# Kernel tuning notes

Hardware: AMD Instinct MI355X
Metric: run time of the kernel (lower is better)

Reference implementation:

```python
import jax, jax.numpy as jnp
import numpy as np
from jax import lax

T, B, D_IN, H, D_OUT = 512, 64, 256, 512, 256


def _lstm_scan(xs, h0, c0, Wih, Whh, b):
    """Standard LSTM over time. xs: [T,B,Din]; returns (hs [T,B,H], hT, cT).
    Gate order i,f,g,o (PyTorch convention)."""
    def step(carry, x_t):
        h, c = carry
        gates = x_t @ Wih.T + h @ Whh.T + b            # [B, 4H]
        i, f, g, o = jnp.split(gates, 4, axis=-1)
        i = jax.nn.sigmoid(i)
        f = jax.nn.sigmoid(f)
        g = jnp.tanh(g)
        o = jax.nn.sigmoid(o)
        c = f * c + i * g
        h = o * jnp.tanh(c)
        return (h, c), h
    (hT, cT), hs = lax.scan(step, (h0, c0), xs)
    return hs, hT, cT


def setup_inputs() -> dict:
    key = jax.random.key(0)
    ks = jax.random.split(key, 10)
    s = 0.05
    return {
        "x": jax.random.normal(ks[0], (T, B, D_IN), jnp.float32),
        "target": jax.random.uniform(ks[1], (T, B, D_OUT), jnp.float32),
        "hidden_state": jnp.zeros((1, B, H), jnp.float32),
        "cell_state": jnp.zeros((1, B, H), jnp.float32),
        "enc_Wih": jax.random.normal(ks[2], (4 * H, D_IN), jnp.float32) * s,
        "enc_Whh": jax.random.normal(ks[3], (4 * H, H), jnp.float32) * s,
        "enc_b": jax.random.normal(ks[4], (4 * H,), jnp.float32) * s,
        "dec_Wih": jax.random.normal(ks[5], (4 * H, D_OUT), jnp.float32) * s,
        "dec_Whh": jax.random.normal(ks[6], (4 * H, H), jnp.float32) * s,
        "dec_b": jax.random.normal(ks[7], (4 * H,), jnp.float32) * s,
        "fc_W": jax.random.normal(ks[8], (D_OUT, H), jnp.float32) * s,
        "fc_b": jax.random.normal(ks[9], (D_OUT,), jnp.float32) * s,
    }


def reference(x, target, hidden_state, cell_state,
              enc_Wih, enc_Whh, enc_b, dec_Wih, dec_Whh, dec_b, fc_W, fc_b):
    # Encoder: consume x, keep final (h, c).
    _, h, c = _lstm_scan(x, hidden_state[0], cell_state[0], enc_Wih, enc_Whh, enc_b)
    # Decoder with teacher_forcing = 1.0: input at step t is target[t-1],
    # step 0 input is zeros (matches torch code's initial x = zeros).
    dec_in = jnp.concatenate([jnp.zeros((1,) + target.shape[1:], target.dtype),
                              target[:-1]], axis=0)          # [T, B, D_OUT]
    hs, _, _ = _lstm_scan(dec_in, h, c, dec_Wih, dec_Whh, dec_b)  # [T, B, H]
    logits = hs @ fc_W.T + fc_b                                   # [T, B, D_OUT]
    return jax.nn.softmax(logits, axis=-1)
```

## Files before the change

kernel.cpp:

```cpp
#include <hip/hip_runtime.h>
#include <math.h>

#define TT 512
#define BB 64
#define DIN 256
#define HH 512
#define DOUT 256

#define RSU 388
#define RSH 776

#define W_HI_OFF 0
#define W_LO_OFF 12416
#define A_HI_OFF 24832
#define A_LO_OFF 31040
#define P_OFF    37248
#define B_OFF    38528
#define C_OFF    38560
#define HST_HI   38688
#define HST_LO   38752
#define SMEM_U32 38816
#define SMEM_BYTES (SMEM_U32*4)

#define FCS 516

typedef _Float16 f16x8 __attribute__((ext_vector_type(8)));
typedef float    f32x4 __attribute__((ext_vector_type(4)));
typedef unsigned u32x4 __attribute__((ext_vector_type(4)));

union H16 { _Float16 f; unsigned short u; };
__device__ __forceinline__ unsigned short f16bits(_Float16 h) { H16 t; t.f = h; return t.u; }

__device__ __forceinline__ void pack2(float x, float y, unsigned& hi, unsigned& lo) {
    _Float16 hx = (_Float16)x, hy = (_Float16)y;
    _Float16 lx = (_Float16)((x - (float)hx) * 2048.0f);
    _Float16 ly = (_Float16)((y - (float)hy) * 2048.0f);
    hi = (unsigned)f16bits(hx) | ((unsigned)f16bits(hy) << 16);
    lo = (unsigned)f16bits(lx) | ((unsigned)f16bits(ly) << 16);
}

__device__ __forceinline__ u32x4 ld16_cohere(const void* p) {
    u32x4 v;
    asm volatile("global_load_dwordx4 %0, %1, off sc0 sc1"
                 : "=&v"(v) : "v"(p) : "memory");
    return v;
}
__device__ __forceinline__ void st16_cohere(void* p, u32x4 v) {
    asm volatile("global_store_dwordx4 %0, %1, off sc0 sc1"
                 :: "v"(p), "v"(v) : "memory");
}

__device__ __forceinline__ void load_w_f16(unsigned* __restrict__ sm32, float* __restrict__ b_l,
                                           const float* __restrict__ Whh,
                                           const float* __restrict__ Wih,
                                           const float* __restrict__ bias,
                                           int u0, int tid) {
    for (int r = 0; r < 48; ++r) {
        int id = tid + 256*r;
        int cc = id / 384;
        int jj = id - cc*384;
        int C  = (cc >> 3)*HH + u0 + (cc & 7);
        float2 v;
        if (jj < 256) v = ((const float2*)(Whh + (size_t)C*HH))[jj];
        else          v = ((const float2*)(Wih + (size_t)C*DIN))[jj - 256];
        unsigned hi, lo;
        pack2(v.x, v.y, hi, lo);
        sm32[W_HI_OFF + cc*RSU + jj] = hi;
        sm32[W_LO_OFF + cc*RSU + jj] = lo;
    }
    if (tid < 32) {
        int C = (tid >> 3)*HH + u0 + (tid & 7);
        b_l[tid] = bias[C];
    }
}

__device__ __forceinline__ void stage_x_f16(unsigned* __restrict__ sm32,
                                            const float* __restrict__ src, int tid) {
    for (int r = 0; r < 4; ++r) {
        int idx4 = tid + 256*r;
        int b = idx4 >> 6, j4 = idx4 & 63;
        float4 v = ((const float4*)(src + (size_t)b*DIN))[j4];
        unsigned h0, l0, h1, l1;
        pack2(v.x, v.y, h0, l0);
        pack2(v.z, v.w, h1, l1);
        int o = b*RSU + 256 + 2*j4;
        sm32[A_HI_OFF + o]     = h0;
        sm32[A_HI_OFF + o + 1] = h1;
        sm32[A_LO_OFF + o]     = l0;
        sm32[A_LO_OFF + o + 1] = l1;
    }
}

__device__ __forceinline__ void stage_x_zero_f16(unsigned* __restrict__ sm32, int tid) {
    for (int r = 0; r < 4; ++r) {
        int idx4 = tid + 256*r;
        int b = idx4 >> 6, j4 = idx4 & 63;
        int o = b*RSU + 256 + 2*j4;
        sm32[A_HI_OFF + o]     = 0u;
        sm32[A_HI_OFF + o + 1] = 0u;
        sm32[A_LO_OFF + o]     = 0u;
        sm32[A_LO_OFF + o + 1] = 0u;
    }
}

__global__ __launch_bounds__(256, 1)
void lstm_persist(const float* __restrict__ x, const float* __restrict__ target,
                  const float* __restrict__ h0, const float* __restrict__ c0,
                  const float* __restrict__ eWih, const float* __restrict__ eWhh,
                  const float* __restrict__ eb,
                  const float* __restrict__ dWih, const float* __restrict__ dWhh,
                  const float* __restrict__ db,
                  float* __restrict__ hs,
                  unsigned short* __restrict__ hbh,
                  unsigned short* __restrict__ hbl,
                  unsigned* __restrict__ bar)
{
    extern __shared__ unsigned sm32[];
    float* p_l = (float*)(sm32 + P_OFF);
    float* b_l = (float*)(sm32 + B_OFF);
    float* c_l = (float*)(sm32 + C_OFF);
    unsigned* hst_hi = sm32 + HST_HI;
    unsigned* hst_lo = sm32 + HST_LO;

    const int tid = (int)threadIdx.x;
    const int xcd = (int)(blockIdx.x & 7);
    const int ib  = xcd >> 1;
    const int sub = xcd & 1;
    const int ij  = (int)(blockIdx.x >> 3) | (sub << 5);
    const int b0  = ib * 16;
    const int u0  = ij * 8;
    unsigned* gflags = bar + ib*64;

    load_w_f16(sm32, b_l, eWhh, eWih, eb, u0, tid);
    if (tid < 128) {
        int b = tid >> 3, u = tid & 7;
        c_l[tid] = c0[(size_t)(b0 + b)*HH + u0 + u];
    }
    stage_x_f16(sm32, x + (size_t)b0*DIN, tid);
    for (int r = 0; r < 8; ++r) {
        int idx4 = tid + 256*r;
        int b = idx4 >> 7, j4 = idx4 & 127;
        float4 v = ((const float4*)(h0 + (size_t)(b0 + b)*HH))[j4];
        unsigned h0p, l0p, h1p, l1p;
        pack2(v.x, v.y, h0p, l0p);
        pack2(v.z, v.w, h1p, l1p);
        int o = b*RSU + 2*j4;
        sm32[A_HI_OFF + o]     = h0p;
        sm32[A_HI_OFF + o + 1] = h1p;
        sm32[A_LO_OFF + o]     = l0p;
        sm32[A_LO_OFF + o + 1] = l1p;
    }
    __syncthreads();

    const int lane = tid & 63;
    const int wid  = tid >> 6;
    const int m    = lane & 15;
    const int q    = lane >> 4;
    const int ct   = wid & 1;
    const int kh   = wid >> 1;

    const _Float16* aH = (const _Float16*)(sm32 + A_HI_OFF);
    const _Float16* aL = (const _Float16*)(sm32 + A_LO_OFF);
    const _Float16* wH = (const _Float16*)(sm32 + W_HI_OFF);
    const _Float16* wL = (const _Float16*)(sm32 + W_LO_OFF);
    const int aoff = m*RSH + q*8;
    const int woff = (ct*16 + m)*RSH + q*8;

    for (int s = 0; s < 1024; ++s) {
        f32x4 Chh = {0.f, 0.f, 0.f, 0.f};
        f32x4 Chl = {0.f, 0.f, 0.f, 0.f};
        f32x4 Clh = {0.f, 0.f, 0.f, 0.f};
        {
            const int ks0 = kh * 12;
            #pragma unroll
            for (int i = 0; i < 12; ++i) {
                const int o = (ks0 + i) * 32;
                f16x8 ah = *(const f16x8*)(aH + aoff + o);
                f16x8 al = *(const f16x8*)(aL + aoff + o);
                f16x8 wh = *(const f16x8*)(wH + woff + o);
                f16x8 wl = *(const f16x8*)(wL + woff + o);
                Chh = __builtin_amdgcn_mfma_f32_16x16x32_f16(ah, wh, Chh, 0, 0, 0);
                Chl = __builtin_amdgcn_mfma_f32_16x16x32_f16(ah, wl, Chl, 0, 0, 0);
                Clh = __builtin_amdgcn_mfma_f32_16x16x32_f16(al, wh, Clh, 0, 0, 0);
            }
        }
        {
            float4 C;
            const float sc = 1.0f / 2048.0f;
            C.x = Chh[0] + (Chl[0] + Clh[0]) * sc;
            C.y = Chh[1] + (Chl[1] + Clh[1]) * sc;
            C.z = Chh[2] + (Chl[2] + Clh[2]) * sc;
            C.w = Chh[3] + (Chl[3] + Clh[3]) * sc;
            *(float4*)(p_l + (ct*2 + kh)*320 + m*20 + q*4) = C;
        }
        __syncthreads();

        float hval = 0.f;
        if (tid < 128) {
            int b = tid >> 3, u = tid & 7;
            float gi = p_l[      u*20 + b] + p_l[320 +      u*20 + b] + b_l[u];
            float gf = p_l[(8+u)*20 + b] + p_l[320 + (8+u)*20 + b] + b_l[8 + u];
            float gg = p_l[640 +   u*20 + b] + p_l[960 +      u*20 + b] + b_l[16 + u];
            float go = p_l[640 + (8+u)*20 + b] + p_l[960 + (8+u)*20 + b] + b_l[24 + u];
            float ii = 1.f / (1.f + expf(-gi));
            float ff = 1.f / (1.f + expf(-gf));
            float g2 = tanhf(gg);
            float oo = 1.f / (1.f + expf(-go));
            float c  = ff * c_l[tid] + ii * g2;
            c_l[tid] = c;
            hval = oo * tanhf(c);
            _Float16 hh = (_Float16)hval;
            _Float16 hl = (_Float16)((hval - (float)hh) * 2048.0f);
            ((unsigned short*)hst_hi)[tid] = f16bits(hh);
            ((unsigned short*)hst_lo)[tid] = f16bits(hl);
        }
        __syncthreads();

        if (tid < 64) {
            if (tid < 32) {
                int b    = tid & 15;
                int isLo = tid >> 4;
                u32x4 v = *(const u32x4*)((isLo ? hst_lo : hst_hi) + b*4);
                unsigned short* base = isLo ? hbl : hbh;
                st16_cohere(base + ((size_t)(((s & 1) ^ 1))*BB + b0 + b)*HH + u0, v);
            }
            asm volatile("s_waitcnt vmcnt(0)" ::: "memory");
            if (tid == 0)
                __hip_atomic_store(&gflags[ij], (unsigned)(s + 1),
                                   __ATOMIC_RELAXED, __HIP_MEMORY_SCOPE_AGENT);
        }

        if (s >= 512 && tid < 128) {
            int b = tid >> 3, u = tid & 7;
            hs[((size_t)(s - 512)*BB + (b0 + b))*HH + (u0 + u)] = hval;
        }
        if (s == 511) load_w_f16(sm32, b_l, dWhh, dWih, db, u0, tid);
        {
            int ns = s + 1;
            if (ns < 1024) {
                if (ns == 512)       stage_x_zero_f16(sm32, tid);
                else if (ns < 512)   stage_x_f16(sm32, x + ((size_t)ns*BB + b0)*DIN, tid);
                else                 stage_x_f16(sm32, target + ((size_t)(ns - 513)*BB + b0)*DOUT, tid);
            }
        }

        if (s < 1023) {
            if (tid < 64) {
                while (true) {
                    unsigned v = __hip_atomic_load(&gflags[tid], __ATOMIC_RELAXED,
                                                   __HIP_MEMORY_SCOPE_AGENT);
                    if (__ballot(v >= (unsigned)(s + 1)) == ~0ull) break;
                    __builtin_amdgcn_s_sleep(1);
                }
            }
            __syncthreads();
            const unsigned short* srcH = hbh + (size_t)((s + 1) & 1)*BB*HH + (size_t)b0*HH;
            const unsigned short* srcL = hbl + (size_t)((s + 1) & 1)*BB*HH + (size_t)b0*HH;
            u32x4 h0v = ld16_cohere((const u32x4*)srcH + tid);
            u32x4 h1v = ld16_cohere((const u32x4*)srcH + tid + 256);
            u32x4 h2v = ld16_cohere((const u32x4*)srcH + tid + 512);
            u32x4 h3v = ld16_cohere((const u32x4*)srcH + tid + 768);
            u32x4 l0v = ld16_cohere((const u32x4*)srcL + tid);
            u32x4 l1v = ld16_cohere((const u32x4*)srcL + tid + 256);
            u32x4 l2v = ld16_cohere((const u32x4*)srcL + tid + 512);
            u32x4 l3v = ld16_cohere((const u32x4*)srcL + tid + 768);
            asm volatile("s_waitcnt vmcnt(0)"
                         : "+v"(h0v), "+v"(h1v), "+v"(h2v), "+v"(h3v),
                           "+v"(l0v), "+v"(l1v), "+v"(l2v), "+v"(l3v) :: "memory");
            {
                int idx, b, j0;
                idx = tid;       b = idx >> 6; j0 = (idx & 63)*4;
                *(u32x4*)(sm32 + A_HI_OFF + b*RSU + j0) = h0v;
                *(u32x4*)(sm32 + A_LO_OFF + b*RSU + j0) = l0v;
                idx = tid + 256; b = idx >> 6; j0 = (idx & 63)*4;
                *(u32x4*)(sm32 + A_HI_OFF + b*RSU + j0) = h1v;
                *(u32x4*)(sm32 + A_LO_OFF + b*RSU + j0) = l1v;
                idx = tid + 512; b = idx >> 6; j0 = (idx & 63)*4;
                *(u32x4*)(sm32 + A_HI_OFF + b*RSU + j0) = h2v;
                *(u32x4*)(sm32 + A_LO_OFF + b*RSU + j0) = l2v;
                idx = tid + 768; b = idx >> 6; j0 = (idx & 63)*4;
                *(u32x4*)(sm32 + A_HI_OFF + b*RSU + j0) = h3v;
                *(u32x4*)(sm32 + A_LO_OFF + b*RSU + j0) = l3v;
            }
        }
        __syncthreads();
    }
}

__global__ __launch_bounds__(256, 1)
void fc_kernel(const float* __restrict__ hs, const float* __restrict__ W,
               const float* __restrict__ bias, float* __restrict__ out)
{
    extern __shared__ float sm[];
    float* hs_l = sm;
    float* w_l  = sm + 16*FCS;

    const int tid = (int)threadIdx.x;
    const int rb = (int)(blockIdx.x >> 3);
    const int cb = (int)(blockIdx.x & 7);

    for (int r = 0; r < 8; ++r) {
        int id = tid + 256*r;
        int b = id >> 7, j = id & 127;
        float4 v = ((const float4*)(hs + (size_t)(rb*16 + b)*HH))[j];
        *(float4*)(hs_l + b*FCS + 4*j) = v;
    }
    for (int r = 0; r < 16; ++r) {
        int id = tid + 256*r;
        int c = id >> 7, j = id & 127;
        float4 v = ((const float4*)(W + (size_t)(cb*32 + c)*HH))[j];
        *(float4*)(w_l + c*FCS + 4*j) = v;
    }
    __syncthreads();

    const int kc = tid & 7, bt = (tid >> 3) & 3, ct = tid >> 5;
    float acc[4][4] = {};
    const float* ap = hs_l + (bt*4)*FCS + 4*kc;
    const float* wp = w_l  + (ct*4)*FCS + 4*kc;
    #pragma unroll 4
    for (int i = 0; i < 16; ++i) {
        float4 av[4], wv[4];
        #pragma unroll
        for (int q = 0; q < 4; ++q) av[q] = *(const float4*)(ap + q*FCS + 32*i);
        #pragma unroll
        for (int q = 0; q < 4; ++q) wv[q] = *(const float4*)(wp + q*FCS + 32*i);
        #pragma unroll
        for (int b2 = 0; b2 < 4; ++b2)
            #pragma unroll
            for (int c2 = 0; c2 < 4; ++c2)
                acc[b2][c2] += av[b2].x*wv[c2].x + av[b2].y*wv[c2].y
                             + av[b2].z*wv[c2].z + av[b2].w*wv[c2].w;
    }
    #pragma unroll
    for (int b2 = 0; b2 < 4; ++b2)
        #pragma unroll
        for (int c2 = 0; c2 < 4; ++c2) {
            float v = acc[b2][c2];
            v += __shfl_xor(v, 1, 64);
            v += __shfl_xor(v, 2, 64);
            v += __shfl_xor(v, 4, 64);
            acc[b2][c2] = v;
        }
    if (kc == 0) {
        #pragma unroll
        for (int b2 = 0; b2 < 4; ++b2)
            #pragma unroll
            for (int c2 = 0; c2 < 4; ++c2) {
                int row = rb*16 + bt*4 + b2;
                int col = cb*32 + ct*4 + c2;
                out[(size_t)row*DOUT + col] = acc[b2][c2] + bias[col];
            }
    }
}

__global__ __launch_bounds__(256, 1)
void softmax_kernel(float* __restrict__ out)
{
    int row  = (int)blockIdx.x * 4 + ((int)threadIdx.x >> 6);
    int lane = (int)threadIdx.x & 63;
    float4 v = ((const float4*)(out + (size_t)row*DOUT))[lane];
    float m = fmaxf(fmaxf(v.x, v.y), fmaxf(v.z, v.w));
    #pragma unroll
    for (int d = 1; d < 64; d <<= 1) m = fmaxf(m, __shfl_xor(m, d, 64));
    float ex = expf(v.x - m), ey = expf(v.y - m), ez = expf(v.z - m), ew = expf(v.w - m);
    float ssum = ex + ey + ez + ew;
    #pragma unroll
    for (int d = 1; d < 64; d <<= 1) ssum += __shfl_xor(ssum, d, 64);
    float inv = 1.f / ssum;
    float4 o = make_float4(ex*inv, ey*inv, ez*inv, ew*inv);
    ((float4*)(out + (size_t)row*DOUT))[lane] = o;
}

__global__ void init_kernel(unsigned* __restrict__ bar)
{
    bar[threadIdx.x] = 0u;
}

extern "C" void kernel_launch(void* const* d_in, const int* in_sizes, int n_in,
                              void* d_out, int out_size, void* d_ws, size_t ws_size,
                              hipStream_t stream) {
    (void)in_sizes; (void)n_in; (void)out_size; (void)ws_size;
    const float* x      = (const float*)d_in[0];
    const float* target = (const float*)d_in[1];
    const float* h0     = (const float*)d_in[2];
    const float* c0     = (const float*)d_in[3];
    const float* eWih   = (const float*)d_in[4];
    const float* eWhh   = (const float*)d_in[5];
    const float* eb     = (const float*)d_in[6];
    const float* dWih   = (const float*)d_in[7];
    const float* dWhh   = (const float*)d_in[8];
    const float* db     = (const float*)d_in[9];
    const float* fcW    = (const float*)d_in[10];
    const float* fcb    = (const float*)d_in[11];
    float* out = (float*)d_out;

    unsigned* bar = (unsigned*)d_ws;
    float* hs = (float*)d_ws + 1024;
    unsigned short* hbh = (unsigned short*)(hs + (size_t)TT*BB*HH);
    unsigned short* hbl = hbh + (size_t)2*BB*HH;

    init_kernel<<<dim3(1), dim3(1024), 0, stream>>>(bar);

    lstm_persist<<<dim3(256), dim3(256), SMEM_BYTES, stream>>>(
        x, target, h0, c0, eWih, eWhh, eb, dWih, dWhh, db, hs, hbh, hbl, bar);

    size_t lds_fc = (size_t)(48*FCS) * sizeof(float);
    fc_kernel<<<dim3(16384), dim3(256), lds_fc, stream>>>(hs, fcW, fcb, out);

    softmax_kernel<<<dim3(8192), dim3(256), 0, stream>>>(out);
}
```

Before: 4.670 ms.

## Replace flag barrier with parity-tagged hidden-state data polling

Drops the per-step global flag barrier (atomic flag store, then a polling loop over 64 flags). Each fp16 hi/lo value of the exchanged hidden state now carries a parity bit in its mantissa LSB, and consumers re-load only the 16-byte chunks whose tags do not yet match the expected parity. This removes one round trip (flag write and flag read) from the critical path of each of the 1024 recurrent steps. In exchange it loses one mantissa bit of the hi part (the lo residual is computed against the tagged value, which compensates) and the lo part, and it relies on 16-byte stores being observed atomically. The init kernel now seeds both buffers with tags matching the initial parity.

```diff
diff --git a/kernel.cpp b/kernel.cpp
--- a/kernel.cpp
+++ b/kernel.cpp
@@ -48,6 +48,13 @@
 __device__ __forceinline__ void st16_cohere(void* p, u32x4 v) {
     asm volatile("global_store_dwordx4 %0, %1, off sc0 sc1"
                  :: "v"(p), "v"(v) : "memory");
+}
+
+__device__ __forceinline__ bool tag_ok(u32x4 v, unsigned par) {
+    unsigned a = v[0] & v[1] & v[2] & v[3];
+    unsigned o = v[0] | v[1] | v[2] | v[3];
+    unsigned x = par ? ~a : o;
+    return (x & 0x00010001u) == 0u;
 }
 
 __device__ __forceinline__ void load_w_f16(unsigned* __restrict__ sm32, float* __restrict__ b_l,
@@ -112,8 +119,7 @@
                   const float* __restrict__ db,
                   float* __restrict__ hs,
                   unsigned short* __restrict__ hbh,
-                  unsigned short* __restrict__ hbl,
-                  unsigned* __restrict__ bar)
+                  unsigned short* __restrict__ hbl)
 {
     extern __shared__ unsigned sm32[];
     float* p_l = (float*)(sm32 + P_OFF);
@@ -129,7 +135,6 @@
     const int ij  = (int)(blockIdx.x >> 3) | (sub << 5);
     const int b0  = ib * 16;
     const int u0  = ij * 8;
-    unsigned* gflags = bar + ib*64;
 
     load_w_f16(sm32, b_l, eWhh, eWih, eb, u0, tid);
     if (tid < 128) {
@@ -195,6 +200,8 @@
         }
         __syncthreads();
 
+        const unsigned par = (unsigned)(((s + 1) >> 1) & 1);
+
         float hval = 0.f;
         if (tid < 128) {
             int b = tid >> 3, u = tid & 7;
@@ -210,24 +217,22 @@
             c_l[tid] = c;
             hval = oo * tanhf(c);
             _Float16 hh = (_Float16)hval;
-            _Float16 hl = (_Float16)((hval - (float)hh) * 2048.0f);
-            ((unsigned short*)hst_hi)[tid] = f16bits(hh);
-            ((unsigned short*)hst_lo)[tid] = f16bits(hl);
+            unsigned uh = ((unsigned)f16bits(hh) & 0xFFFEu) | par;
+            H16 th; th.u = (unsigned short)uh;
+            _Float16 hl = (_Float16)((hval - (float)th.f) * 2048.0f);
+            unsigned ul = ((unsigned)f16bits(hl) & 0xFFFEu) | par;
+            ((unsigned short*)hst_hi)[tid] = (unsigned short)uh;
+            ((unsigned short*)hst_lo)[tid] = (unsigned short)ul;
         }
         __syncthreads();
 
-        if (tid < 64) {
-            if (tid < 32) {
-                int b    = tid & 15;
-                int isLo = tid >> 4;
-                u32x4 v = *(const u32x4*)((isLo ? hst_lo : hst_hi) + b*4);
-                unsigned short* base = isLo ? hbl : hbh;
-                st16_cohere(base + ((size_t)(((s & 1) ^ 1))*BB + b0 + b)*HH + u0, v);
-            }
+        if (tid < 32) {
             asm volatile("s_waitcnt vmcnt(0)" ::: "memory");
-            if (tid == 0)
-                __hip_atomic_store(&gflags[ij], (unsigned)(s + 1),
-                                   __ATOMIC_RELAXED, __HIP_MEMORY_SCOPE_AGENT);
+            int b    = tid & 15;
+            int isLo = tid >> 4;
+            u32x4 v = *(const u32x4*)((isLo ? hst_lo : hst_hi) + b*4);
+            unsigned short* base = isLo ? hbl : hbh;
+            st16_cohere(base + ((size_t)(((s & 1) ^ 1))*BB + b0 + b)*HH + u0, v);
         }
 
         if (s >= 512 && tid < 128) {
@@ -245,28 +250,32 @@
         }
 
         if (s < 1023) {
-            if (tid < 64) {
-                while (true) {
-                    unsigned v = __hip_atomic_load(&gflags[tid], __ATOMIC_RELAXED,
-                                                   __HIP_MEMORY_SCOPE_AGENT);
-                    if (__ballot(v >= (unsigned)(s + 1)) == ~0ull) break;
-                    __builtin_amdgcn_s_sleep(1);
-                }
-            }
-            __syncthreads();
             const unsigned short* srcH = hbh + (size_t)((s + 1) & 1)*BB*HH + (size_t)b0*HH;
             const unsigned short* srcL = hbl + (size_t)((s + 1) & 1)*BB*HH + (size_t)b0*HH;
-            u32x4 h0v = ld16_cohere((const u32x4*)srcH + tid);
-            u32x4 h1v = ld16_cohere((const u32x4*)srcH + tid + 256);
-            u32x4 h2v = ld16_cohere((const u32x4*)srcH + tid + 512);
-            u32x4 h3v = ld16_cohere((const u32x4*)srcH + tid + 768);
-            u32x4 l0v = ld16_cohere((const u32x4*)srcL + tid);
-            u32x4 l1v = ld16_cohere((const u32x4*)srcL + tid + 256);
-            u32x4 l2v = ld16_cohere((const u32x4*)srcL + tid + 512);
-            u32x4 l3v = ld16_cohere((const u32x4*)srcL + tid + 768);
-            asm volatile("s_waitcnt vmcnt(0)"
-                         : "+v"(h0v), "+v"(h1v), "+v"(h2v), "+v"(h3v),
-                           "+v"(l0v), "+v"(l1v), "+v"(l2v), "+v"(l3v) :: "memory");
+            u32x4 h0v = {0,0,0,0}, h1v = {0,0,0,0}, h2v = {0,0,0,0}, h3v = {0,0,0,0};
+            u32x4 l0v = {0,0,0,0}, l1v = {0,0,0,0}, l2v = {0,0,0,0}, l3v = {0,0,0,0};
+            unsigned pend = 0xFFu;
+            do {
+                if (pend & 0x01u) h0v = ld16_cohere((const u32x4*)srcH + tid);
+                if (pend & 0x02u) h1v = ld16_cohere((const u32x4*)srcH + tid + 256);
+                if (pend & 0x04u) h2v = ld16_cohere((const u32x4*)srcH + tid + 512);
+                if (pend & 0x08u) h3v = ld16_cohere((const u32x4*)srcH + tid + 768);
+                if (pend & 0x10u) l0v = ld16_cohere((const u32x4*)srcL + tid);
+                if (pend & 0x20u) l1v = ld16_cohere((const u32x4*)srcL + tid + 256);
+                if (pend & 0x40u) l2v = ld16_cohere((const u32x4*)srcL + tid + 512);
+                if (pend & 0x80u) l3v = ld16_cohere((const u32x4*)srcL + tid + 768);
+                asm volatile("s_waitcnt vmcnt(0)"
+                             : "+v"(h0v), "+v"(h1v), "+v"(h2v), "+v"(h3v),
+                               "+v"(l0v), "+v"(l1v), "+v"(l2v), "+v"(l3v) :: "memory");
+                if (tag_ok(h0v, par)) pend &= ~0x01u;
+                if (tag_ok(h1v, par)) pend &= ~0x02u;
+                if (tag_ok(h2v, par)) pend &= ~0x04u;
+                if (tag_ok(h3v, par)) pend &= ~0x08u;
+                if (tag_ok(l0v, par)) pend &= ~0x10u;
+                if (tag_ok(l1v, par)) pend &= ~0x20u;
+                if (tag_ok(l2v, par)) pend &= ~0x40u;
+                if (tag_ok(l3v, par)) pend &= ~0x80u;
+            } while (pend);
             {
                 int idx, b, j0;
                 idx = tid;       b = idx >> 6; j0 = (idx & 63)*4;
@@ -371,9 +380,14 @@
     ((float4*)(out + (size_t)row*DOUT))[lane] = o;
 }
 
-__global__ void init_kernel(unsigned* __restrict__ bar)
+__global__ void init_kernel(unsigned* __restrict__ hbh32, unsigned* __restrict__ hbl32)
 {
-    bar[threadIdx.x] = 0u;
+    int i = (int)blockIdx.x * 256 + (int)threadIdx.x;
+    unsigned* base = (i < 8192) ? hbh32 : hbl32;
+    int j = (i & 8191) * 4;
+    unsigned val = (j < 16384) ? 0u : 0x00010001u;
+    u32x4 v = {val, val, val, val};
+    *(u32x4*)(base + j) = v;
 }
 
 extern "C" void kernel_launch(void* const* d_in, const int* in_sizes, int n_in,
@@ -394,15 +408,14 @@
     const float* fcb    = (const float*)d_in[11];
     float* out = (float*)d_out;
 
-    unsigned* bar = (unsigned*)d_ws;
     float* hs = (float*)d_ws + 1024;
     unsigned short* hbh = (unsigned short*)(hs + (size_t)TT*BB*HH);
     unsigned short* hbl = hbh + (size_t)2*BB*HH;
 
-    init_kernel<<<dim3(1), dim3(1024), 0, stream>>>(bar);
+    init_kernel<<<dim3(64), dim3(256), 0, stream>>>((unsigned*)hbh, (unsigned*)hbl);
 
     lstm_persist<<<dim3(256), dim3(256), SMEM_BYTES, stream>>>(
-        x, target, h0, c0, eWih, eWhh, eb, dWih, dWhh, db, hs, hbh, hbl, bar);
+        x, target, h0, c0, eWih, eWhh, eb, dWih, dWhh, db, hs, hbh, hbl);
 
     size_t lds_fc = (size_t)(48*FCS) * sizeof(float);
     fc_kernel<<<dim3(16384), dim3(256), lds_fc, stream>>>(hs, fcW, fcb, out);
```

New measurement: 4.021 ms. -13.9%, faster.
